# Optimization experiments

Hardware: AMD Instinct MI355X
Metric: run time of the kernel (lower is better)

The kernel has to match this reference:

```python
import jax, jax.numpy as jnp
import numpy as np

D = 48


def setup_inputs() -> dict:
    key = jax.random.key(0)
    k1, k2, k3, k4, k5 = jax.random.split(key, 5)
    B, N, d = 4, 512, D
    x = jax.random.normal(k1, (B, N, d), dtype=jnp.float32)
    # Linear(2d, 2d) and Linear(2d, d); stored as (in, out) so y = x @ W + b
    s1 = 1.0 / np.sqrt(2 * d)
    W1 = jax.random.uniform(k2, (2 * d, 2 * d), dtype=jnp.float32, minval=-s1, maxval=s1)
    b1 = jax.random.uniform(k3, (2 * d,), dtype=jnp.float32, minval=-s1, maxval=s1)
    W2 = jax.random.uniform(k4, (2 * d, d), dtype=jnp.float32, minval=-s1, maxval=s1)
    b2 = jax.random.uniform(k5, (d,), dtype=jnp.float32, minval=-s1, maxval=s1)
    return {"x": x, "W1": W1, "b1": b1, "W2": W2, "b2": b2}


def reference(x, W1, b1, W2, b2):
    B, N, d = x.shape
    # pairwise concat: [B, N, N, 2d] with (i, j) = (x_i, x_j)
    xi = jnp.broadcast_to(x[:, :, None, :], (B, N, N, d))
    xj = jnp.broadcast_to(x[:, None, :, :], (B, N, N, d))
    cat = jnp.concatenate([xi, xj], axis=-1)
    h = jax.nn.gelu(cat @ W1 + b1, approximate=False)  # torch GELU is exact erf form
    p = h @ W2 + b2  # [B, N, N, d]
    mask = jnp.triu(jnp.ones((N, N), dtype=bool), 1)  # j > i masked
    p = jnp.where(mask[None, :, :, None], 0.0, p)
    w = jnp.sqrt(jnp.sum(p * p, axis=-1))  # frobenius norm over feature dim -> [B, N, N]
    w = jnp.where(mask[None, :, :], -1e9, w)
    w = jax.nn.softmax(w, axis=-1)[..., None]  # softmax over j
    return jnp.sum(w * p, axis=2)  # [B, N, d]
```

## Files before the change

### kernel.cpp

```cpp
#include <hip/hip_runtime.h>
#include <hip/hip_bf16.h>
#include <math.h>

#define DD 48
#define NN 512
#define TWO_D 96
#define ROWS 2048

typedef __attribute__((ext_vector_type(8))) short bf16x8;
typedef __attribute__((ext_vector_type(4))) float f32x4;

__device__ __forceinline__ float gelu_fast(float u) {
    const float u2 = u * u;
    const float yn = u * fmaf(u2, -0.10295347f, -2.3022587f);
    const float e = __builtin_amdgcn_exp2f(yn);
    return u * __builtin_amdgcn_rcpf(1.0f + e);
}

__global__ __launch_bounds__(256) void precompute_kernel(
        const float* __restrict__ x,
        const float* __restrict__ W1,
        const float* __restrict__ b1,
        const float* __restrict__ W2,
        float* __restrict__ Aout,
        float* __restrict__ Bout,
        __hip_bfloat16* __restrict__ W2T) {
    if (blockIdx.x == ROWS / 4) {
        for (int idx = threadIdx.x; idx < DD * TWO_D; idx += 256) {
            const int f = idx / TWO_D;
            const int k = idx - f * TWO_D;
            W2T[idx] = __float2bfloat16(W2[k * DD + f]);
        }
        return;
    }
    const int wave = threadIdx.x >> 6;
    const int lane = threadIdx.x & 63;
    const int row = blockIdx.x * 4 + wave;
    __shared__ float xs[4][DD];
    if (threadIdx.x < 4 * DD)
        xs[threadIdx.x / DD][threadIdx.x % DD] = x[blockIdx.x * 4 * DD + threadIdx.x];
    __syncthreads();
    for (int t = lane; t < TWO_D; t += 64) {
        float a0 = 0.f, a1 = 0.f;
#pragma unroll 8
        for (int k = 0; k < DD; ++k) {
            const float xv = xs[wave][k];
            a0 = fmaf(xv, W1[k * TWO_D + t], a0);
            a1 = fmaf(xv, W1[(DD + k) * TWO_D + t], a1);
        }
        Aout[row * TWO_D + t] = a0 + b1[t];
        Bout[row * TWO_D + t] = a1;
    }
}

__global__ __launch_bounds__(256) void pair_softmax_kernel(
        const float* __restrict__ Arow,
        const float* __restrict__ Brow,
        const __hip_bfloat16* __restrict__ W2T,
        const float* __restrict__ b2,
        float* __restrict__ out) {
    const int e = blockIdx.x >> 8;
    const int p = blockIdx.x & 255;
    const int base = (e & 1) ? ((e >> 1) << 6) : (448 - ((e >> 1) << 6));
    const int off = (e & 1) ? (63 - (p >> 2)) : (p >> 2);
    const int i = base + off;
    const int row = (p & 3) * NN + i;

    const int tid = threadIdx.x;
    const int wave = tid >> 6;
    const int lane = tid & 63;
    const int n = lane & 15;
    const int q = lane >> 4;
    const int q8 = q * 8;

    const float* __restrict__ Bbase = Brow + (size_t)(row - i) * TWO_D;

    bf16x8 bfrag[3][3];
#pragma unroll
    for (int t = 0; t < 3; ++t)
#pragma unroll
        for (int ks = 0; ks < 3; ++ks)
            bfrag[t][ks] = *(const bf16x8*)&W2T[(t * 16 + n) * TWO_D + ks * 32 + q8];
    float b2v[3];
#pragma unroll
    for (int t = 0; t < 3; ++t) b2v[t] = b2[t * 16 + n];

    float av[3][8];
#pragma unroll
    for (int ks = 0; ks < 3; ++ks) {
        const float4 a0 = *(const float4*)&Arow[(size_t)row * TWO_D + ks * 32 + q8];
        const float4 a1 = *(const float4*)&Arow[(size_t)row * TWO_D + ks * 32 + q8 + 4];
        av[ks][0] = a0.x; av[ks][1] = a0.y; av[ks][2] = a0.z; av[ks][3] = a0.w;
        av[ks][4] = a1.x; av[ks][5] = a1.y; av[ks][6] = a1.z; av[ks][7] = a1.w;
    }

    float l_run = 0.f;
    float o_run[3] = {0.f, 0.f, 0.f};

    const int nchunks = (i + 16) >> 4;
    const ptrdiff_t cstep = 64 * TWO_D;

    const float* __restrict__ Bj = Bbase + (size_t)(wave * 16 + n) * TWO_D;
    float4 pb[6];
    if (wave < nchunks) {
#pragma unroll
        for (int ks = 0; ks < 3; ++ks) {
            pb[2 * ks]     = *(const float4*)&Bj[ks * 32 + q8];
            pb[2 * ks + 1] = *(const float4*)&Bj[ks * 32 + q8 + 4];
        }
    }

    for (int c = wave; c < nchunks; c += 4) {
        const int j0 = c << 4;
        const bool hn = (c + 4) < nchunks;
        const float* __restrict__ Bjn = Bj + cstep;

        f32x4 acc[3] = {{0.f,0.f,0.f,0.f},{0.f,0.f,0.f,0.f},{0.f,0.f,0.f,0.f}};
#pragma unroll
        for (int ks = 0; ks < 3; ++ks) {
            const float4 bv0 = pb[2 * ks];
            const float4 bv1 = pb[2 * ks + 1];
            if (hn) {
                pb[2 * ks]     = *(const float4*)&Bjn[ks * 32 + q8];
                pb[2 * ks + 1] = *(const float4*)&Bjn[ks * 32 + q8 + 4];
            }
            float h[8];
            h[0] = gelu_fast(av[ks][0] + bv0.x);
            h[1] = gelu_fast(av[ks][1] + bv0.y);
            h[2] = gelu_fast(av[ks][2] + bv0.z);
            h[3] = gelu_fast(av[ks][3] + bv0.w);
            h[4] = gelu_fast(av[ks][4] + bv1.x);
            h[5] = gelu_fast(av[ks][5] + bv1.y);
            h[6] = gelu_fast(av[ks][6] + bv1.z);
            h[7] = gelu_fast(av[ks][7] + bv1.w);
            union { bf16x8 v; __hip_bfloat162 h2[4]; } af;
#pragma unroll
            for (int pp = 0; pp < 4; ++pp)
                af.h2[pp] = __float22bfloat162_rn(make_float2(h[2 * pp], h[2 * pp + 1]));
            acc[0] = __builtin_amdgcn_mfma_f32_16x16x32_bf16(af.v, bfrag[0][ks], acc[0], 0, 0, 0);
            acc[1] = __builtin_amdgcn_mfma_f32_16x16x32_bf16(af.v, bfrag[1][ks], acc[1], 0, 0, 0);
            acc[2] = __builtin_amdgcn_mfma_f32_16x16x32_bf16(af.v, bfrag[2][ks], acc[2], 0, 0, 0);
        }
        Bj = Bjn;

        float pv[3][4];
        float ss[4];
#pragma unroll
        for (int r = 0; r < 4; ++r) {
            float s = 0.f;
#pragma unroll
            for (int t = 0; t < 3; ++t) {
                const float pz = acc[t][r] + b2v[t];
                pv[t][r] = pz;
                s = fmaf(pz, pz, s);
            }
            ss[r] = s;
        }
#pragma unroll
        for (int d = 1; d <= 8; d <<= 1) {
#pragma unroll
            for (int r = 0; r < 4; ++r) ss[r] += __shfl_xor(ss[r], d);
        }
        float ew[4];
#pragma unroll
        for (int r = 0; r < 4; ++r) {
            const int j = j0 + 4 * q + r;
            ew[r] = (j <= i) ? __expf(sqrtf(ss[r])) : 0.f;
        }
        l_run += (ew[0] + ew[1]) + (ew[2] + ew[3]);
#pragma unroll
        for (int t = 0; t < 3; ++t)
            o_run[t] += ew[0]*pv[t][0] + ew[1]*pv[t][1] + ew[2]*pv[t][2] + ew[3]*pv[t][3];
    }

    l_run += __shfl_xor(l_run, 16);
    l_run += __shfl_xor(l_run, 32);
#pragma unroll
    for (int t = 0; t < 3; ++t) {
        o_run[t] += __shfl_xor(o_run[t], 16);
        o_run[t] += __shfl_xor(o_run[t], 32);
    }
    __shared__ float lred[4];
    __shared__ float ored[4][DD];
    if (lane < 16) {
#pragma unroll
        for (int t = 0; t < 3; ++t) ored[wave][t * 16 + n] = o_run[t];
    }
    if (lane == 0) lred[wave] = l_run;
    __syncthreads();
    if (tid < DD) {
        float L = 0.f, O = 0.f;
#pragma unroll
        for (int wv = 0; wv < 4; ++wv) {
            L += lred[wv];
            O += ored[wv][tid];
        }
        out[row * DD + tid] = O / L;
    }
}

extern "C" void kernel_launch(void* const* d_in, const int* in_sizes, int n_in,
                              void* d_out, int out_size, void* d_ws, size_t ws_size,
                              hipStream_t stream) {
    const float* x  = (const float*)d_in[0];
    const float* W1 = (const float*)d_in[1];
    const float* b1 = (const float*)d_in[2];
    const float* W2 = (const float*)d_in[3];
    const float* b2 = (const float*)d_in[4];
    float* outp = (float*)d_out;

    float* A  = (float*)d_ws;
    float* Bb = A + ROWS * TWO_D;
    __hip_bfloat16* W2T = (__hip_bfloat16*)(Bb + ROWS * TWO_D);

    precompute_kernel<<<ROWS / 4 + 1, 256, 0, stream>>>(x, W1, b1, W2, A, Bb, W2T);
    pair_softmax_kernel<<<ROWS, 256, 0, stream>>>(A, Bb, W2T, b2, outp);
}
```

Measured before the change: 104.5 us.

## Replace rolling B prefetch with paired-chunk loads and add occupancy hint

The per-iteration software prefetch of the next chunk's B rows is replaced by a loop that issues loads for two chunks up front and then processes both back to back. It also adds a launch_bounds minimum-blocks hint of 4. The intent is to put more independent loads in flight per iteration and to cap register use for higher occupancy. In exchange, loads for the next pair are no longer overlapped with the current pair's compute, and the register cap could cause spills.

New measurement: 113.3 us. +8.5%, slower.

```diff
diff --git a/kernel.cpp b/kernel.cpp
--- a/kernel.cpp
+++ b/kernel.cpp
@@ -53,7 +53,7 @@
     }
 }
 
-__global__ __launch_bounds__(256) void pair_softmax_kernel(
+__global__ __launch_bounds__(256, 4) void pair_softmax_kernel(
         const float* __restrict__ Arow,
         const float* __restrict__ Brow,
         const __hip_bfloat16* __restrict__ W2T,
@@ -98,32 +98,23 @@
     float o_run[3] = {0.f, 0.f, 0.f};
 
     const int nchunks = (i + 16) >> 4;
-    const ptrdiff_t cstep = 64 * TWO_D;
-
-    const float* __restrict__ Bj = Bbase + (size_t)(wave * 16 + n) * TWO_D;
-    float4 pb[6];
-    if (wave < nchunks) {
+
+    auto loadB = [&](int c, float4* bv) {
+        const float* __restrict__ Bj = Bbase + (size_t)((c << 4) + n) * TWO_D;
 #pragma unroll
         for (int ks = 0; ks < 3; ++ks) {
-            pb[2 * ks]     = *(const float4*)&Bj[ks * 32 + q8];
-            pb[2 * ks + 1] = *(const float4*)&Bj[ks * 32 + q8 + 4];
-        }
-    }
-
-    for (int c = wave; c < nchunks; c += 4) {
+            bv[2 * ks]     = *(const float4*)&Bj[ks * 32 + q8];
+            bv[2 * ks + 1] = *(const float4*)&Bj[ks * 32 + q8 + 4];
+        }
+    };
+
+    auto do_chunk = [&](int c, const float4* bv) {
         const int j0 = c << 4;
-        const bool hn = (c + 4) < nchunks;
-        const float* __restrict__ Bjn = Bj + cstep;
-
         f32x4 acc[3] = {{0.f,0.f,0.f,0.f},{0.f,0.f,0.f,0.f},{0.f,0.f,0.f,0.f}};
 #pragma unroll
         for (int ks = 0; ks < 3; ++ks) {
-            const float4 bv0 = pb[2 * ks];
-            const float4 bv1 = pb[2 * ks + 1];
-            if (hn) {
-                pb[2 * ks]     = *(const float4*)&Bjn[ks * 32 + q8];
-                pb[2 * ks + 1] = *(const float4*)&Bjn[ks * 32 + q8 + 4];
-            }
+            const float4 bv0 = bv[2 * ks];
+            const float4 bv1 = bv[2 * ks + 1];
             float h[8];
             h[0] = gelu_fast(av[ks][0] + bv0.x);
             h[1] = gelu_fast(av[ks][1] + bv0.y);
@@ -141,8 +132,6 @@
             acc[1] = __builtin_amdgcn_mfma_f32_16x16x32_bf16(af.v, bfrag[1][ks], acc[1], 0, 0, 0);
             acc[2] = __builtin_amdgcn_mfma_f32_16x16x32_bf16(af.v, bfrag[2][ks], acc[2], 0, 0, 0);
         }
-        Bj = Bjn;
-
         float pv[3][4];
         float ss[4];
 #pragma unroll
@@ -171,6 +160,15 @@
 #pragma unroll
         for (int t = 0; t < 3; ++t)
             o_run[t] += ew[0]*pv[t][0] + ew[1]*pv[t][1] + ew[2]*pv[t][2] + ew[3]*pv[t][3];
+    };
+
+    for (int c = wave; c < nchunks; c += 8) {
+        const bool has2 = (c + 4) < nchunks;
+        float4 bvA[6], bvB[6];
+        loadB(c, bvA);
+        if (has2) loadB(c + 4, bvB);
+        do_chunk(c, bvA);
+        if (has2) do_chunk(c + 4, bvB);
     }
 
     l_run += __shfl_xor(l_run, 16);
```

## Transpose MFMA operands, replace GELU with erf polynomial, add occupancy hint

Applied to the files above, without the earlier changes.

Swaps the MFMA operand order so each lane holds outputs for one pair index j across four features. The per-pair squared-norm reduction then needs only two cross-lane shuffles, and one exp per lane instead of four. The shuffle reductions of the output accumulators move out of the hot loop to a single epilogue, at the cost of more accumulator registers (12 instead of 3). The sigmoid-based GELU approximation is replaced by a clamped odd polynomial erf approximation with no transcendental calls, and a min-blocks-per-CU launch bound of 4 is added.

After: 118.0 us. 13.0% more time.

```diff
diff --git a/kernel.cpp b/kernel.cpp
--- a/kernel.cpp
+++ b/kernel.cpp
@@ -10,11 +10,15 @@
 typedef __attribute__((ext_vector_type(8))) short bf16x8;
 typedef __attribute__((ext_vector_type(4))) float f32x4;
 
-__device__ __forceinline__ float gelu_fast(float u) {
-    const float u2 = u * u;
-    const float yn = u * fmaf(u2, -0.10295347f, -2.3022587f);
-    const float e = __builtin_amdgcn_exp2f(yn);
-    return u * __builtin_amdgcn_rcpf(1.0f + e);
+__device__ __forceinline__ float gelu_poly(float u) {
+    const float uc = fminf(fmaxf(u, -3.5777f), 3.5777f);
+    const float v = uc * uc;
+    float E = fmaf(v, -1.04448e-6f, 4.61896e-5f);
+    E = fmaf(v, E, -8.62284e-4f);
+    E = fmaf(v, E, 9.22138e-3f);
+    E = fmaf(v, E, -6.58353e-2f);
+    E = fmaf(v, E, 3.98855e-1f);
+    return u * fmaf(uc, E, 0.5f);
 }
 
 __global__ __launch_bounds__(256) void precompute_kernel(
@@ -53,7 +57,7 @@
     }
 }
 
-__global__ __launch_bounds__(256) void pair_softmax_kernel(
+__global__ __launch_bounds__(256, 4) void pair_softmax_kernel(
         const float* __restrict__ Arow,
         const float* __restrict__ Brow,
         const __hip_bfloat16* __restrict__ W2T,
@@ -81,9 +85,11 @@
 #pragma unroll
         for (int ks = 0; ks < 3; ++ks)
             bfrag[t][ks] = *(const bf16x8*)&W2T[(t * 16 + n) * TWO_D + ks * 32 + q8];
-    float b2v[3];
-#pragma unroll
-    for (int t = 0; t < 3; ++t) b2v[t] = b2[t * 16 + n];
+    float b2v[3][4];
+#pragma unroll
+    for (int t = 0; t < 3; ++t)
+#pragma unroll
+        for (int r = 0; r < 4; ++r) b2v[t][r] = b2[t * 16 + 4 * q + r];
 
     float av[3][8];
 #pragma unroll
@@ -95,7 +101,7 @@
     }
 
     float l_run = 0.f;
-    float o_run[3] = {0.f, 0.f, 0.f};
+    float o_run[3][4] = {{0.f,0.f,0.f,0.f},{0.f,0.f,0.f,0.f},{0.f,0.f,0.f,0.f}};
 
     const int nchunks = (i + 16) >> 4;
     const ptrdiff_t cstep = 64 * TWO_D;
@@ -125,66 +131,64 @@
                 pb[2 * ks + 1] = *(const float4*)&Bjn[ks * 32 + q8 + 4];
             }
             float h[8];
-            h[0] = gelu_fast(av[ks][0] + bv0.x);
-            h[1] = gelu_fast(av[ks][1] + bv0.y);
-            h[2] = gelu_fast(av[ks][2] + bv0.z);
-            h[3] = gelu_fast(av[ks][3] + bv0.w);
-            h[4] = gelu_fast(av[ks][4] + bv1.x);
-            h[5] = gelu_fast(av[ks][5] + bv1.y);
-            h[6] = gelu_fast(av[ks][6] + bv1.z);
-            h[7] = gelu_fast(av[ks][7] + bv1.w);
-            union { bf16x8 v; __hip_bfloat162 h2[4]; } af;
+            h[0] = gelu_poly(av[ks][0] + bv0.x);
+            h[1] = gelu_poly(av[ks][1] + bv0.y);
+            h[2] = gelu_poly(av[ks][2] + bv0.z);
+            h[3] = gelu_poly(av[ks][3] + bv0.w);
+            h[4] = gelu_poly(av[ks][4] + bv1.x);
+            h[5] = gelu_poly(av[ks][5] + bv1.y);
+            h[6] = gelu_poly(av[ks][6] + bv1.z);
+            h[7] = gelu_poly(av[ks][7] + bv1.w);
+            union { bf16x8 v; __hip_bfloat162 h2[4]; } hf;
 #pragma unroll
             for (int pp = 0; pp < 4; ++pp)
-                af.h2[pp] = __float22bfloat162_rn(make_float2(h[2 * pp], h[2 * pp + 1]));
-            acc[0] = __builtin_amdgcn_mfma_f32_16x16x32_bf16(af.v, bfrag[0][ks], acc[0], 0, 0, 0);
-            acc[1] = __builtin_amdgcn_mfma_f32_16x16x32_bf16(af.v, bfrag[1][ks], acc[1], 0, 0, 0);
-            acc[2] = __builtin_amdgcn_mfma_f32_16x16x32_bf16(af.v, bfrag[2][ks], acc[2], 0, 0, 0);
+                hf.h2[pp] = __float22bfloat162_rn(make_float2(h[2 * pp], h[2 * pp + 1]));
+            acc[0] = __builtin_amdgcn_mfma_f32_16x16x32_bf16(bfrag[0][ks], hf.v, acc[0], 0, 0, 0);
+            acc[1] = __builtin_amdgcn_mfma_f32_16x16x32_bf16(bfrag[1][ks], hf.v, acc[1], 0, 0, 0);
+            acc[2] = __builtin_amdgcn_mfma_f32_16x16x32_bf16(bfrag[2][ks], hf.v, acc[2], 0, 0, 0);
         }
         Bj = Bjn;
 
         float pv[3][4];
-        float ss[4];
-#pragma unroll
-        for (int r = 0; r < 4; ++r) {
-            float s = 0.f;
-#pragma unroll
-            for (int t = 0; t < 3; ++t) {
-                const float pz = acc[t][r] + b2v[t];
+        float ss = 0.f;
+#pragma unroll
+        for (int t = 0; t < 3; ++t)
+#pragma unroll
+            for (int r = 0; r < 4; ++r) {
+                const float pz = acc[t][r] + b2v[t][r];
                 pv[t][r] = pz;
-                s = fmaf(pz, pz, s);
+                ss = fmaf(pz, pz, ss);
             }
-            ss[r] = s;
-        }
-#pragma unroll
-        for (int d = 1; d <= 8; d <<= 1) {
-#pragma unroll
-            for (int r = 0; r < 4; ++r) ss[r] += __shfl_xor(ss[r], d);
-        }
-        float ew[4];
-#pragma unroll
-        for (int r = 0; r < 4; ++r) {
-            const int j = j0 + 4 * q + r;
-            ew[r] = (j <= i) ? __expf(sqrtf(ss[r])) : 0.f;
-        }
-        l_run += (ew[0] + ew[1]) + (ew[2] + ew[3]);
-#pragma unroll
-        for (int t = 0; t < 3; ++t)
-            o_run[t] += ew[0]*pv[t][0] + ew[1]*pv[t][1] + ew[2]*pv[t][2] + ew[3]*pv[t][3];
-    }
-
-    l_run += __shfl_xor(l_run, 16);
-    l_run += __shfl_xor(l_run, 32);
-#pragma unroll
-    for (int t = 0; t < 3; ++t) {
-        o_run[t] += __shfl_xor(o_run[t], 16);
-        o_run[t] += __shfl_xor(o_run[t], 32);
+        ss += __shfl_xor(ss, 16);
+        ss += __shfl_xor(ss, 32);
+        const int j = j0 + n;
+        const float ew = (j <= i)
+            ? __builtin_amdgcn_exp2f(sqrtf(ss) * 1.44269504f) : 0.f;
+        l_run += ew;
+#pragma unroll
+        for (int t = 0; t < 3; ++t)
+#pragma unroll
+            for (int r = 0; r < 4; ++r)
+                o_run[t][r] = fmaf(ew, pv[t][r], o_run[t][r]);
+    }
+
+#pragma unroll
+    for (int d = 1; d <= 8; d <<= 1) {
+        l_run += __shfl_xor(l_run, d);
+#pragma unroll
+        for (int t = 0; t < 3; ++t)
+#pragma unroll
+            for (int r = 0; r < 4; ++r)
+                o_run[t][r] += __shfl_xor(o_run[t][r], d);
     }
     __shared__ float lred[4];
     __shared__ float ored[4][DD];
-    if (lane < 16) {
-#pragma unroll
-        for (int t = 0; t < 3; ++t) ored[wave][t * 16 + n] = o_run[t];
+    if (n == 0) {
+#pragma unroll
+        for (int t = 0; t < 3; ++t)
+#pragma unroll
+            for (int r = 0; r < 4; ++r)
+                ored[wave][t * 16 + 4 * q + r] = o_run[t][r];
     }
     if (lane == 0) lred[wave] = l_run;
     __syncthreads();
```
